# Performance work log

Measured on AMD Instinct MI355X. Metric: run time of the kernel, lower is better.

The kernel has to match this reference:

```python
import jax, jax.numpy as jnp
import numpy as np

B, N, C = 2, 1024, 768
H = 12            # num_heads
HP = 24           # H_prime
HD = C // H       # head_dim = 64
KS = 3            # local conv kernel size
SCALE = HD ** -0.5


def setup_inputs() -> dict:
    key = jax.random.key(0)
    ks = jax.random.split(key, 9)
    s = lambda fan_in: 1.0 / np.sqrt(fan_in)
    return {
        "x": jax.random.normal(ks[0], (B, N, C), jnp.float32),
        "W_qk": jax.random.normal(ks[1], (2 * C, C), jnp.float32) * s(C),
        "W_v": jax.random.normal(ks[2], (C, C), jnp.float32) * s(C),
        "W_exp": jax.random.normal(ks[3], (HP, H), jnp.float32) * s(H),      # 1x1 conv H->HP
        "W_loc": jax.random.normal(ks[4], (HP, 1, KS, KS), jnp.float32) * s(KS * KS),  # depthwise 3x3
        "b_loc": jnp.zeros((HP,), jnp.float32),
        "W_red": jax.random.normal(ks[5], (H, HP), jnp.float32) * s(HP),    # 1x1 conv HP->H
        "W_proj": jax.random.normal(ks[6], (C, C), jnp.float32) * s(C),
        "b_proj": jnp.zeros((C,), jnp.float32),
    }


def _forward(x, W_qk, W_v, W_exp, W_loc, b_loc, W_red, W_proj, b_proj):
    b, n, c = x.shape
    # Attention: qk projection -> (2,B,H,N,HD)
    qk = (x @ W_qk.T).reshape(b, n, 2, H, HD).transpose(2, 0, 3, 1, 4)
    q, k = qk[0], qk[1]                                   # (B,H,N,HD)
    v = (x @ W_v.T).reshape(b, n, H, HD).transpose(0, 2, 1, 3)  # (B,H,N,HD)
    attn = jax.nn.softmax(jnp.einsum('bhnd,bhmd->bhnm', q, k) * SCALE, axis=-1)  # (B,H,N,N)

    # TokenSelector: conv-based reweighting of the attention map
    A_exp = jnp.einsum('oi,binm->bonm', W_exp, attn)      # 1x1 expand -> (B,HP,N,N)
    A_loc = jax.lax.conv_general_dilated(
        A_exp, W_loc, window_strides=(1, 1), padding='SAME',
        dimension_numbers=('NCHW', 'OIHW', 'NCHW'),
        feature_group_count=HP) + b_loc[None, :, None, None]
    A_loc = jax.nn.relu(A_loc)
    A_red = jnp.einsum('oi,binm->bonm', W_red, A_loc) * SCALE  # (B,H,N,N)
    attn2 = jax.nn.softmax(A_red, axis=-1)

    out = jnp.einsum('bhnm,bhmd->bhnd', attn2, v)         # (B,H,N,HD)
    out = out.transpose(0, 2, 1, 3).reshape(b, n, c)      # (B,N,C)
    out = out @ W_proj.T + b_proj
    return out, A_exp


def reference(x, W_qk, W_v, W_exp, W_loc, b_loc, W_red, W_proj, b_proj):
    return _forward(x, W_qk, W_v, W_exp, W_loc, b_loc, W_red, W_proj, b_proj)
```

## Files before the change

kernel.cpp:

```cpp
#include <hip/hip_runtime.h>
#include <math.h>

#define BB    2
#define NN    1024
#define CC    768
#define HH    12
#define HPP   24
#define HD    64
#define SCALE 0.125f

typedef float fvec4 __attribute__((ext_vector_type(4)));

#define SEG   (2*1024*768)
#define QOFF  0
#define KOFF  (SEG)
#define VOFF  (2*SEG)
#define HOFF  (3*SEG)

__global__ __launch_bounds__(256)
void qkv_gemm(const float* __restrict__ x, const float* __restrict__ Wqk,
              const float* __restrict__ Wv, float* __restrict__ ws)
{
    __shared__ float As[16][68];
    __shared__ float Bs[16][68];
    float* qtok = ws + QOFF;
    float* kt   = ws + KOFF;
    float* vws  = ws + VOFF;

    const int tid  = threadIdx.x;
    const int bn   = blockIdx.x;
    const int bm   = blockIdx.y;
    const int tx   = tid & 15, ty = tid >> 4;
    const int lrow = tid >> 2;
    const int lk   = (tid & 3) << 2;

    const int jrow = bn * 64 + lrow;
    const float* Bsrc = (jrow < 1536) ? (Wqk + (size_t)jrow * 768)
                                      : (Wv  + (size_t)(jrow - 1536) * 768);
    const float* Asrc = x + (size_t)(bm * 64 + lrow) * 768;

    float c[4][4] = {};

    for (int k0 = 0; k0 < 768; k0 += 16) {
        float4 av = *(const float4*)(Asrc + k0 + lk);
        float4 bv = *(const float4*)(Bsrc + k0 + lk);
        __syncthreads();
        As[lk+0][lrow] = av.x; As[lk+1][lrow] = av.y;
        As[lk+2][lrow] = av.z; As[lk+3][lrow] = av.w;
        Bs[lk+0][lrow] = bv.x; Bs[lk+1][lrow] = bv.y;
        Bs[lk+2][lrow] = bv.z; Bs[lk+3][lrow] = bv.w;
        __syncthreads();
#pragma unroll
        for (int kk = 0; kk < 16; ++kk) {
            float a[4], b[4];
#pragma unroll
            for (int i = 0; i < 4; ++i) a[i] = As[kk][ty*4 + i];
#pragma unroll
            for (int j = 0; j < 4; ++j) b[j] = Bs[kk][tx*4 + j];
#pragma unroll
            for (int i = 0; i < 4; ++i)
#pragma unroll
                for (int j = 0; j < 4; ++j)
                    c[i][j] = fmaf(a[i], b[j], c[i][j]);
        }
    }

#pragma unroll
    for (int i = 0; i < 4; ++i) {
        const int t = bm*64 + ty*4 + i;
        const int b = t >> 10, n = t & 1023;
#pragma unroll
        for (int j = 0; j < 4; ++j) {
            const int col = bn*64 + tx*4 + j;
            const float val = c[i][j];
            if (col < 768) {
                qtok[(size_t)t*768 + col] = val;
            } else if (col < 1536) {
                const int p = col - 768;
                kt[((size_t)(b*768 + p))*NN + n] = val;
            } else {
                const int p = col - 1536;
                vws[(((size_t)b*HH + (p >> 6))*NN + n)*HD + (p & 63)] = val;
            }
        }
    }
}

__global__ __launch_bounds__(256, 4)
void attn_expand(const float* __restrict__ qtok, const float* __restrict__ kt,
                 const float* __restrict__ Wexp, float* __restrict__ aexp)
{
    __shared__ __align__(16) float qs[2*CC];
    __shared__ float wexp_s[HPP * HH];
    __shared__ float smax[2][HH * 4];
    __shared__ float ssum[2][HH * 4];

    const int tid  = threadIdx.x;
    const int lane = tid & 63, wid = tid >> 6;
    const int x    = blockIdx.x & 7;
    const int b    = x >> 2;
    const int np   = ((x & 3) << 7) | (blockIdx.x >> 3);
    const int n0   = np << 1;
    const int m4   = tid;

    const fvec4* qsrc = (const fvec4*)(qtok + (size_t)(b*NN + n0) * CC);
    ((fvec4*)qs)[tid] = qsrc[tid];
    if (tid < 128) ((fvec4*)qs)[256 + tid] = qsrc[256 + tid];
    for (int i2 = tid; i2 < HPP*HH; i2 += 256) wexp_s[i2] = Wexp[i2];
    __syncthreads();

    fvec4 l0[HH], l1[HH];
#pragma unroll
    for (int h = 0; h < HH; ++h) {
        fvec4 a0 = {0.f,0.f,0.f,0.f}, a1 = {0.f,0.f,0.f,0.f};
        const fvec4* kr = ((const fvec4*)kt) + (size_t)(b*768 + h*64) * 256 + m4;
        const float* q0p = qs + h*64;
        const float* q1p = qs + CC + h*64;
#pragma unroll 8
        for (int d = 0; d < 64; ++d) {
            const fvec4 kv = kr[(size_t)d * 256];
            const float qa = q0p[d];
            const float qb = q1p[d];
            a0.x = fmaf(kv.x, qa, a0.x); a0.y = fmaf(kv.y, qa, a0.y);
            a0.z = fmaf(kv.z, qa, a0.z); a0.w = fmaf(kv.w, qa, a0.w);
            a1.x = fmaf(kv.x, qb, a1.x); a1.y = fmaf(kv.y, qb, a1.y);
            a1.z = fmaf(kv.z, qb, a1.z); a1.w = fmaf(kv.w, qb, a1.w);
        }
        l0[h].x = a0.x*SCALE; l0[h].y = a0.y*SCALE;
        l0[h].z = a0.z*SCALE; l0[h].w = a0.w*SCALE;
        l1[h].x = a1.x*SCALE; l1[h].y = a1.y*SCALE;
        l1[h].z = a1.z*SCALE; l1[h].w = a1.w*SCALE;
    }

#pragma unroll
    for (int h = 0; h < HH; ++h) {
        float t0 = fmaxf(fmaxf(l0[h].x, l0[h].y), fmaxf(l0[h].z, l0[h].w));
        float t1 = fmaxf(fmaxf(l1[h].x, l1[h].y), fmaxf(l1[h].z, l1[h].w));
#pragma unroll
        for (int off = 32; off > 0; off >>= 1) {
            t0 = fmaxf(t0, __shfl_xor(t0, off, 64));
            t1 = fmaxf(t1, __shfl_xor(t1, off, 64));
        }
        if (lane == 0) { smax[0][h*4 + wid] = t0; smax[1][h*4 + wid] = t1; }
    }
    __syncthreads();

#pragma unroll
    for (int h = 0; h < HH; ++h) {
        const float m0 = fmaxf(fmaxf(smax[0][h*4+0], smax[0][h*4+1]),
                               fmaxf(smax[0][h*4+2], smax[0][h*4+3]));
        const float m1 = fmaxf(fmaxf(smax[1][h*4+0], smax[1][h*4+1]),
                               fmaxf(smax[1][h*4+2], smax[1][h*4+3]));
        l0[h].x = __expf(l0[h].x - m0); l0[h].y = __expf(l0[h].y - m0);
        l0[h].z = __expf(l0[h].z - m0); l0[h].w = __expf(l0[h].w - m0);
        l1[h].x = __expf(l1[h].x - m1); l1[h].y = __expf(l1[h].y - m1);
        l1[h].z = __expf(l1[h].z - m1); l1[h].w = __expf(l1[h].w - m1);
        float s0 = (l0[h].x + l0[h].y) + (l0[h].z + l0[h].w);
        float s1 = (l1[h].x + l1[h].y) + (l1[h].z + l1[h].w);
#pragma unroll
        for (int off = 32; off > 0; off >>= 1) {
            s0 += __shfl_xor(s0, off, 64);
            s1 += __shfl_xor(s1, off, 64);
        }
        if (lane == 0) { ssum[0][h*4 + wid] = s0; ssum[1][h*4 + wid] = s1; }
    }
    __syncthreads();

#pragma unroll
    for (int h = 0; h < HH; ++h) {
        const float i0 = 1.f / (ssum[0][h*4+0] + ssum[0][h*4+1] +
                                ssum[0][h*4+2] + ssum[0][h*4+3]);
        const float i1 = 1.f / (ssum[1][h*4+0] + ssum[1][h*4+1] +
                                ssum[1][h*4+2] + ssum[1][h*4+3]);
        l0[h].x *= i0; l0[h].y *= i0; l0[h].z *= i0; l0[h].w *= i0;
        l1[h].x *= i1; l1[h].y *= i1; l1[h].z *= i1; l1[h].w *= i1;
    }

    fvec4* ab = ((fvec4*)aexp) + ((size_t)b*HPP*NN + n0) * 256;
#pragma unroll 4
    for (int o = 0; o < HPP; ++o) {
        fvec4 e0 = {0.f,0.f,0.f,0.f}, e1 = {0.f,0.f,0.f,0.f};
#pragma unroll
        for (int h = 0; h < HH; ++h) {
            const float w = wexp_s[o*HH + h];
            e0.x = fmaf(w, l0[h].x, e0.x); e0.y = fmaf(w, l0[h].y, e0.y);
            e0.z = fmaf(w, l0[h].z, e0.z); e0.w = fmaf(w, l0[h].w, e0.w);
            e1.x = fmaf(w, l1[h].x, e1.x); e1.y = fmaf(w, l1[h].y, e1.y);
            e1.z = fmaf(w, l1[h].z, e1.z); e1.w = fmaf(w, l1[h].w, e1.w);
        }
        fvec4* p0 = ab + (size_t)o * NN * 256 + m4;
        __builtin_nontemporal_store(e0, p0);
        __builtin_nontemporal_store(e1, p0 + 256);
    }
}

__global__ __launch_bounds__(512, 4)
void conv_red_pv(const float* __restrict__ aexp, const float* __restrict__ Wloc,
                 const float* __restrict__ bloc, const float* __restrict__ Wred,
                 const float* __restrict__ vws, float* __restrict__ hout)
{
    __shared__ __align__(16) float probs[8][NN];
    __shared__ float redbuf[2][HH][4];

    const int tid  = threadIdx.x;
    const int lane = tid & 63;
    const int w    = tid >> 6;
    const int tk   = w >> 2;
    const int wq   = w & 3;
    const int t    = tid & 255;

    const int x  = blockIdx.x & 7;
    const int b  = x >> 2;
    const int np = ((x & 3) << 7) | (blockIdx.x >> 3);
    const int n0 = np << 1;
    const int n  = n0 + tk;

    const bool rv0 = n > 0, rv2 = n < NN - 1;

    float4 acc[HH];
#pragma unroll
    for (int i = 0; i < HH; ++i) acc[i] = make_float4(0.f,0.f,0.f,0.f);

    auto loadch = [&](int o, float4 ld[3], float hl[3], float hr[3]) {
        const float* cb = aexp + ((size_t)(b*HPP + o) * NN + (size_t)(n-1)) * NN;
#pragma unroll
        for (int r = 0; r < 3; ++r) {
            const bool ok = (r == 0) ? rv0 : (r == 2 ? rv2 : true);
            const float* rp = cb + (size_t)r * NN;
            if (ok) {
                ld[r] = ((const float4*)rp)[t];
                hl[r] = (lane == 0  && wq > 0) ? rp[4*t - 1] : 0.f;
                hr[r] = (lane == 63 && wq < 3) ? rp[4*t + 4] : 0.f;
            } else {
                ld[r] = make_float4(0.f,0.f,0.f,0.f);
                hl[r] = 0.f; hr[r] = 0.f;
            }
        }
    };

    float4 ld[3]; float hl[3], hr[3];
    loadch(0, ld, hl, hr);

    for (int o = 0; o < HPP; ++o) {
        float4 l2[3]; float h2l[3], h2r[3];
        if (o < HPP-1) loadch(o+1, l2, h2l, h2r);

        const float* wl = Wloc + o*9;
        const float  bb = bloc[o];
        float v0 = bb, v1 = bb, v2 = bb, v3 = bb;
#pragma unroll
        for (int r = 0; r < 3; ++r) {
            const float w0 = wl[r*3+0], w1 = wl[r*3+1], w2 = wl[r*3+2];
            const float4 c = ld[r];
            float lf = __shfl_up(c.w, 1, 64);
            float rt = __shfl_down(c.x, 1, 64);
            if (lane == 0)  lf = hl[r];
            if (lane == 63) rt = hr[r];
            v0 = fmaf(w0, lf,  v0); v0 = fmaf(w1, c.x, v0); v0 = fmaf(w2, c.y, v0);
            v1 = fmaf(w0, c.x, v1); v1 = fmaf(w1, c.y, v1); v1 = fmaf(w2, c.z, v1);
            v2 = fmaf(w0, c.y, v2); v2 = fmaf(w1, c.z, v2); v2 = fmaf(w2, c.w, v2);
            v3 = fmaf(w0, c.z, v3); v3 = fmaf(w1, c.w, v3); v3 = fmaf(w2, rt,  v3);
        }
        v0 = fmaxf(v0, 0.f); v1 = fmaxf(v1, 0.f);
        v2 = fmaxf(v2, 0.f); v3 = fmaxf(v3, 0.f);
#pragma unroll
        for (int i = 0; i < HH; ++i) {
            const float wr = Wred[i*HPP + o];
            acc[i].x = fmaf(wr, v0, acc[i].x);
            acc[i].y = fmaf(wr, v1, acc[i].y);
            acc[i].z = fmaf(wr, v2, acc[i].z);
            acc[i].w = fmaf(wr, v3, acc[i].w);
        }
        if (o < HPP-1) {
#pragma unroll
            for (int r = 0; r < 3; ++r) { ld[r]=l2[r]; hl[r]=h2l[r]; hr[r]=h2r[r]; }
        }
    }
#pragma unroll
    for (int i = 0; i < HH; ++i) {
        acc[i].x *= SCALE; acc[i].y *= SCALE;
        acc[i].z *= SCALE; acc[i].w *= SCALE;
    }

#pragma unroll
    for (int i = 0; i < HH; ++i) {
        float tm = fmaxf(fmaxf(acc[i].x, acc[i].y), fmaxf(acc[i].z, acc[i].w));
#pragma unroll
        for (int off = 32; off > 0; off >>= 1) tm = fmaxf(tm, __shfl_xor(tm, off, 64));
        if (lane == 0) redbuf[tk][i][wq] = tm;
    }
    __syncthreads();
    float mh[HH];
#pragma unroll
    for (int i = 0; i < HH; ++i)
        mh[i] = fmaxf(fmaxf(redbuf[tk][i][0], redbuf[tk][i][1]),
                      fmaxf(redbuf[tk][i][2], redbuf[tk][i][3]));
    __syncthreads();

#pragma unroll
    for (int i = 0; i < HH; ++i) {
        acc[i].x = __expf(acc[i].x - mh[i]);
        acc[i].y = __expf(acc[i].y - mh[i]);
        acc[i].z = __expf(acc[i].z - mh[i]);
        acc[i].w = __expf(acc[i].w - mh[i]);
        float s = (acc[i].x + acc[i].y) + (acc[i].z + acc[i].w);
#pragma unroll
        for (int off = 32; off > 0; off >>= 1) s += __shfl_xor(s, off, 64);
        if (lane == 0) redbuf[tk][i][wq] = s;
    }
    __syncthreads();
#pragma unroll
    for (int i = 0; i < HH; ++i) {
        const float inv = 1.f / (redbuf[tk][i][0] + redbuf[tk][i][1] +
                                 redbuf[tk][i][2] + redbuf[tk][i][3]);
        acc[i].x *= inv; acc[i].y *= inv; acc[i].z *= inv; acc[i].w *= inv;
    }

    const int hq = w >> 1;
    const int dh = w & 1;
    const int mg = lane >> 3;
    const int dq = lane & 7;

    for (int g = 0; g < 3; ++g) {
        __syncthreads();
#pragma unroll
        for (int q2 = 0; q2 < 4; ++q2)
            ((float4*)&probs[q2*2 + tk][0])[t] = acc[4*g + q2];
        __syncthreads();

        const int h = 4*g + hq;
        const float4* vp = ((const float4*)vws)
                         + ((size_t)(b*HH + h) * NN) * 16 + dh*8 + dq;
        const float* p0 = &probs[hq*2 + 0][0] + mg;
        const float* p1 = &probs[hq*2 + 1][0] + mg;
        float4 a0 = make_float4(0.f,0.f,0.f,0.f);
        float4 a1 = make_float4(0.f,0.f,0.f,0.f);
#pragma unroll 8
        for (int m0 = 0; m0 < NN; m0 += 8) {
            const float  pa = p0[m0];
            const float  pb = p1[m0];
            const float4 vv = vp[(size_t)(m0 + mg) * 16];
            a0.x = fmaf(pa, vv.x, a0.x); a0.y = fmaf(pa, vv.y, a0.y);
            a0.z = fmaf(pa, vv.z, a0.z); a0.w = fmaf(pa, vv.w, a0.w);
            a1.x = fmaf(pb, vv.x, a1.x); a1.y = fmaf(pb, vv.y, a1.y);
            a1.z = fmaf(pb, vv.z, a1.z); a1.w = fmaf(pb, vv.w, a1.w);
        }
#pragma unroll
        for (int off = 8; off < 64; off <<= 1) {
            a0.x += __shfl_xor(a0.x, off, 64); a0.y += __shfl_xor(a0.y, off, 64);
            a0.z += __shfl_xor(a0.z, off, 64); a0.w += __shfl_xor(a0.w, off, 64);
            a1.x += __shfl_xor(a1.x, off, 64); a1.y += __shfl_xor(a1.y, off, 64);
            a1.z += __shfl_xor(a1.z, off, 64); a1.w += __shfl_xor(a1.w, off, 64);
        }
        if (mg == 0) {
            ((float4*)(hout + ((size_t)(b*NN + n0    ) * CC) + h*HD))[dh*8 + dq] = a0;
            ((float4*)(hout + ((size_t)(b*NN + n0 + 1) * CC) + h*HD))[dh*8 + dq] = a1;
        }
    }
}

__global__ __launch_bounds__(256)
void proj_gemm(const float* __restrict__ A, const float* __restrict__ Wp,
               const float* __restrict__ bias, float* __restrict__ out)
{
    __shared__ float As[16][68];
    __shared__ float Bs[16][68];

    const int tid  = threadIdx.x;
    const int bn   = blockIdx.x;
    const int bm   = blockIdx.y;
    const int tx   = tid & 15, ty = tid >> 4;
    const int lrow = tid >> 2;
    const int lk   = (tid & 3) << 2;

    const float* Asrc = A  + (size_t)(bm*64 + lrow) * 768;
    const float* Bsrc = Wp + (size_t)(bn*64 + lrow) * 768;

    float c[4][4] = {};

    for (int k0 = 0; k0 < 768; k0 += 16) {
        float4 av = *(const float4*)(Asrc + k0 + lk);
        float4 bv = *(const float4*)(Bsrc + k0 + lk);
        __syncthreads();
        As[lk+0][lrow] = av.x; As[lk+1][lrow] = av.y;
        As[lk+2][lrow] = av.z; As[lk+3][lrow] = av.w;
        Bs[lk+0][lrow] = bv.x; Bs[lk+1][lrow] = bv.y;
        Bs[lk+2][lrow] = bv.z; Bs[lk+3][lrow] = bv.w;
        __syncthreads();
#pragma unroll
        for (int kk = 0; kk < 16; ++kk) {
            float a[4], b[4];
#pragma unroll
            for (int i = 0; i < 4; ++i) a[i] = As[kk][ty*4 + i];
#pragma unroll
            for (int j = 0; j < 4; ++j) b[j] = Bs[kk][tx*4 + j];
#pragma unroll
            for (int i = 0; i < 4; ++i)
#pragma unroll
                for (int j = 0; j < 4; ++j)
                    c[i][j] = fmaf(a[i], b[j], c[i][j]);
        }
    }

#pragma unroll
    for (int i = 0; i < 4; ++i) {
        const int t = bm*64 + ty*4 + i;
#pragma unroll
        for (int j = 0; j < 4; ++j) {
            const int col = bn*64 + tx*4 + j;
            out[(size_t)t*768 + col] = c[i][j] + bias[col];
        }
    }
}

extern "C" void kernel_launch(void* const* d_in, const int* in_sizes, int n_in,
                              void* d_out, int out_size, void* d_ws, size_t ws_size,
                              hipStream_t stream)
{
    const float* x     = (const float*)d_in[0];
    const float* Wqk   = (const float*)d_in[1];
    const float* Wv    = (const float*)d_in[2];
    const float* Wexp  = (const float*)d_in[3];
    const float* Wloc  = (const float*)d_in[4];
    const float* bloc  = (const float*)d_in[5];
    const float* Wred  = (const float*)d_in[6];
    const float* Wproj = (const float*)d_in[7];
    const float* bproj = (const float*)d_in[8];

    float* out  = (float*)d_out;
    float* aexp = out + (size_t)SEG;
    float* ws   = (float*)d_ws;

    qkv_gemm   <<<dim3(36, 32), 256, 0, stream>>>(x, Wqk, Wv, ws);
    attn_expand<<<dim3(BB * NN / 2), 256, 0, stream>>>(ws + QOFF, ws + KOFF, Wexp, aexp);
    conv_red_pv<<<dim3(BB * NN / 2), 512, 0, stream>>>(aexp, Wloc, bloc, Wred,
                                                       ws + VOFF, ws + HOFF);
    proj_gemm  <<<dim3(12, 32), 256, 0, stream>>>(ws + HOFF, Wproj, bproj, out);
}
```

Before: 768.9 us.

## Enlarge GEMM tiles to 128x64 with double-buffered LDS and vector stores

```diff
diff --git a/kernel.cpp b/kernel.cpp
--- a/kernel.cpp
+++ b/kernel.cpp
@@ -17,76 +17,109 @@
 #define VOFF  (2*SEG)
 #define HOFF  (3*SEG)
 
+#define ASTR 132
+#define BSTR 68
+
 __global__ __launch_bounds__(256)
 void qkv_gemm(const float* __restrict__ x, const float* __restrict__ Wqk,
               const float* __restrict__ Wv, float* __restrict__ ws)
 {
-    __shared__ float As[16][68];
-    __shared__ float Bs[16][68];
+    __shared__ float As[2][16*ASTR];
+    __shared__ float Bs[2][16*BSTR];
     float* qtok = ws + QOFF;
     float* kt   = ws + KOFF;
     float* vws  = ws + VOFF;
 
-    const int tid  = threadIdx.x;
-    const int bn   = blockIdx.x;
-    const int bm   = blockIdx.y;
-    const int tx   = tid & 15, ty = tid >> 4;
-    const int lrow = tid >> 2;
-    const int lk   = (tid & 3) << 2;
-
-    const int jrow = bn * 64 + lrow;
-    const float* Bsrc = (jrow < 1536) ? (Wqk + (size_t)jrow * 768)
-                                      : (Wv  + (size_t)(jrow - 1536) * 768);
-    const float* Asrc = x + (size_t)(bm * 64 + lrow) * 768;
-
-    float c[4][4] = {};
-
-    for (int k0 = 0; k0 < 768; k0 += 16) {
-        float4 av = *(const float4*)(Asrc + k0 + lk);
-        float4 bv = *(const float4*)(Bsrc + k0 + lk);
+    const int tid = threadIdx.x;
+    const int bn  = blockIdx.x;
+    const int bm  = blockIdx.y;
+    const int tx  = tid & 15, ty = tid >> 4;
+
+    const int am  = tid >> 1, ak = (tid & 1) * 8;
+    const int bnr = tid >> 2, bk = (tid & 3) * 4;
+
+    const float* Ap = x + (size_t)(bm*128 + am) * 768 + ak;
+    const int jrow  = bn*64 + bnr;
+    const float* Bp = (jrow < 1536) ? (Wqk + (size_t)jrow * 768 + bk)
+                                    : (Wv  + (size_t)(jrow - 1536) * 768 + bk);
+
+    float acc[8][4] = {};
+
+    float4 a0 = *(const float4*)(Ap);
+    float4 a1 = *(const float4*)(Ap + 4);
+    float4 bv = *(const float4*)(Bp);
+#pragma unroll
+    for (int j = 0; j < 4; ++j) {
+        As[0][(ak+j)*ASTR + am]   = ((const float*)&a0)[j];
+        As[0][(ak+4+j)*ASTR + am] = ((const float*)&a1)[j];
+        Bs[0][(bk+j)*BSTR + bnr]  = ((const float*)&bv)[j];
+    }
+    __syncthreads();
+
+    for (int t = 0; t < 48; ++t) {
+        const int cur = t & 1;
+        if (t < 47) {
+            a0 = *(const float4*)(Ap + (t+1)*16);
+            a1 = *(const float4*)(Ap + (t+1)*16 + 4);
+            bv = *(const float4*)(Bp + (t+1)*16);
+        }
+        const float* Asb = As[cur];
+        const float* Bsb = Bs[cur];
+#pragma unroll
+        for (int kk = 0; kk < 16; ++kk) {
+            float a[8], b[4];
+#pragma unroll
+            for (int i = 0; i < 8; ++i) a[i] = Asb[kk*ASTR + ty*8 + i];
+#pragma unroll
+            for (int j = 0; j < 4; ++j) b[j] = Bsb[kk*BSTR + tx*4 + j];
+#pragma unroll
+            for (int i = 0; i < 8; ++i)
+#pragma unroll
+                for (int j = 0; j < 4; ++j)
+                    acc[i][j] = fmaf(a[i], b[j], acc[i][j]);
+        }
+        if (t < 47) {
+#pragma unroll
+            for (int j = 0; j < 4; ++j) {
+                As[cur^1][(ak+j)*ASTR + am]   = ((const float*)&a0)[j];
+                As[cur^1][(ak+4+j)*ASTR + am] = ((const float*)&a1)[j];
+                Bs[cur^1][(bk+j)*BSTR + bnr]  = ((const float*)&bv)[j];
+            }
+        }
         __syncthreads();
-        As[lk+0][lrow] = av.x; As[lk+1][lrow] = av.y;
-        As[lk+2][lrow] = av.z; As[lk+3][lrow] = av.w;
-        Bs[lk+0][lrow] = bv.x; Bs[lk+1][lrow] = bv.y;
-        Bs[lk+2][lrow] = bv.z; Bs[lk+3][lrow] = bv.w;
-        __syncthreads();
-#pragma unroll
-        for (int kk = 0; kk < 16; ++kk) {
-            float a[4], b[4];
-#pragma unroll
-            for (int i = 0; i < 4; ++i) a[i] = As[kk][ty*4 + i];
-#pragma unroll
-            for (int j = 0; j < 4; ++j) b[j] = Bs[kk][tx*4 + j];
-#pragma unroll
-            for (int i = 0; i < 4; ++i)
-#pragma unroll
-                for (int j = 0; j < 4; ++j)
-                    c[i][j] = fmaf(a[i], b[j], c[i][j]);
-        }
-    }
-
-#pragma unroll
-    for (int i = 0; i < 4; ++i) {
-        const int t = bm*64 + ty*4 + i;
-        const int b = t >> 10, n = t & 1023;
-#pragma unroll
-        for (int j = 0; j < 4; ++j) {
-            const int col = bn*64 + tx*4 + j;
-            const float val = c[i][j];
-            if (col < 768) {
-                qtok[(size_t)t*768 + col] = val;
-            } else if (col < 1536) {
-                const int p = col - 768;
-                kt[((size_t)(b*768 + p))*NN + n] = val;
-            } else {
-                const int p = col - 1536;
-                vws[(((size_t)b*HH + (p >> 6))*NN + n)*HD + (p & 63)] = val;
-            }
+    }
+
+    const int colbase = bn*64 + tx*4;
+    if (colbase < 768) {
+#pragma unroll
+        for (int i = 0; i < 8; ++i) {
+            const int trow = bm*128 + ty*8 + i;
+            float4 o = {acc[i][0], acc[i][1], acc[i][2], acc[i][3]};
+            *(float4*)(qtok + (size_t)trow*768 + colbase) = o;
+        }
+    } else if (colbase < 1536) {
+        const int p = colbase - 768;
+#pragma unroll
+        for (int i = 0; i < 8; ++i) {
+            const int trow = bm*128 + ty*8 + i;
+            const int b = trow >> 10, n = trow & 1023;
+#pragma unroll
+            for (int j = 0; j < 4; ++j)
+                kt[((size_t)(b*768 + p + j))*NN + n] = acc[i][j];
+        }
+    } else {
+        const int p = colbase - 1536;
+#pragma unroll
+        for (int i = 0; i < 8; ++i) {
+            const int trow = bm*128 + ty*8 + i;
+            const int b = trow >> 10, n = trow & 1023;
+            float4 o = {acc[i][0], acc[i][1], acc[i][2], acc[i][3]};
+            *(float4*)(vws + (((size_t)b*HH + (p >> 6))*NN + n)*HD + (p & 63)) = o;
         }
     }
 }
 
-__global__ __launch_bounds__(256, 4)
+__global__ __launch_bounds__(256, 2)
 void attn_expand(const float* __restrict__ qtok, const float* __restrict__ kt,
                  const float* __restrict__ Wexp, float* __restrict__ aexp)
 {
@@ -194,7 +227,7 @@
     }
 }
 
-__global__ __launch_bounds__(512, 4)
+__global__ __launch_bounds__(512, 2)
 void conv_red_pv(const float* __restrict__ aexp, const float* __restrict__ Wloc,
                  const float* __restrict__ bloc, const float* __restrict__ Wred,
                  const float* __restrict__ vws, float* __restrict__ hout)
@@ -363,53 +396,74 @@
 void proj_gemm(const float* __restrict__ A, const float* __restrict__ Wp,
                const float* __restrict__ bias, float* __restrict__ out)
 {
-    __shared__ float As[16][68];
-    __shared__ float Bs[16][68];
-
-    const int tid  = threadIdx.x;
-    const int bn   = blockIdx.x;
-    const int bm   = blockIdx.y;
-    const int tx   = tid & 15, ty = tid >> 4;
-    const int lrow = tid >> 2;
-    const int lk   = (tid & 3) << 2;
-
-    const float* Asrc = A  + (size_t)(bm*64 + lrow) * 768;
-    const float* Bsrc = Wp + (size_t)(bn*64 + lrow) * 768;
-
-    float c[4][4] = {};
-
-    for (int k0 = 0; k0 < 768; k0 += 16) {
-        float4 av = *(const float4*)(Asrc + k0 + lk);
-        float4 bv = *(const float4*)(Bsrc + k0 + lk);
+    __shared__ float As[2][16*ASTR];
+    __shared__ float Bs[2][16*BSTR];
+
+    const int tid = threadIdx.x;
+    const int bn  = blockIdx.x;
+    const int bm  = blockIdx.y;
+    const int tx  = tid & 15, ty = tid >> 4;
+
+    const int am  = tid >> 1, ak = (tid & 1) * 8;
+    const int bnr = tid >> 2, bk = (tid & 3) * 4;
+
+    const float* Ap = A  + (size_t)(bm*128 + am) * 768 + ak;
+    const float* Bp = Wp + (size_t)(bn*64 + bnr) * 768 + bk;
+
+    float acc[8][4] = {};
+
+    float4 a0 = *(const float4*)(Ap);
+    float4 a1 = *(const float4*)(Ap + 4);
+    float4 bv = *(const float4*)(Bp);
+#pragma unroll
+    for (int j = 0; j < 4; ++j) {
+        As[0][(ak+j)*ASTR + am]   = ((const float*)&a0)[j];
+        As[0][(ak+4+j)*ASTR + am] = ((const float*)&a1)[j];
+        Bs[0][(bk+j)*BSTR + bnr]  = ((const float*)&bv)[j];
+    }
+    __syncthreads();
+
+    for (int t = 0; t < 48; ++t) {
+        const int cur = t & 1;
+        if (t < 47) {
+            a0 = *(const float4*)(Ap + (t+1)*16);
+            a1 = *(const float4*)(Ap + (t+1)*16 + 4);
+            bv = *(const float4*)(Bp + (t+1)*16);
+        }
+        const float* Asb = As[cur];
+        const float* Bsb = Bs[cur];
+#pragma unroll
+        for (int kk = 0; kk < 16; ++kk) {
+            float a[8], b[4];
+#pragma unroll
+            for (int i = 0; i < 8; ++i) a[i] = Asb[kk*ASTR + ty*8 + i];
+#pragma unroll
+            for (int j = 0; j < 4; ++j) b[j] = Bsb[kk*BSTR + tx*4 + j];
+#pragma unroll
+            for (int i = 0; i < 8; ++i)
+#pragma unroll
+                for (int j = 0; j < 4; ++j)
+                    acc[i][j] = fmaf(a[i], b[j], acc[i][j]);
+        }
+        if (t < 47) {
+#pragma unroll
+            for (int j = 0; j < 4; ++j) {
+                As[cur^1][(ak+j)*ASTR + am]   = ((const float*)&a0)[j];
+                As[cur^1][(ak+4+j)*ASTR + am] = ((const float*)&a1)[j];
+                Bs[cur^1][(bk+j)*BSTR + bnr]  = ((const float*)&bv)[j];
+            }
+        }
         __syncthreads();
-        As[lk+0][lrow] = av.x; As[lk+1][lrow] = av.y;
-        As[lk+2][lrow] = av.z; As[lk+3][lrow] = av.w;
-        Bs[lk+0][lrow] = bv.x; Bs[lk+1][lrow] = bv.y;
-        Bs[lk+2][lrow] = bv.z; Bs[lk+3][lrow] = bv.w;
-        __syncthreads();
-#pragma unroll
-        for (int kk = 0; kk < 16; ++kk) {
-            float a[4], b[4];
-#pragma unroll
-            for (int i = 0; i < 4; ++i) a[i] = As[kk][ty*4 + i];
-#pragma unroll
-            for (int j = 0; j < 4; ++j) b[j] = Bs[kk][tx*4 + j];
-#pragma unroll
-            for (int i = 0; i < 4; ++i)
-#pragma unroll
-                for (int j = 0; j < 4; ++j)
-                    c[i][j] = fmaf(a[i], b[j], c[i][j]);
-        }
-    }
-
-#pragma unroll
-    for (int i = 0; i < 4; ++i) {
-        const int t = bm*64 + ty*4 + i;
-#pragma unroll
-        for (int j = 0; j < 4; ++j) {
-            const int col = bn*64 + tx*4 + j;
-            out[(size_t)t*768 + col] = c[i][j] + bias[col];
-        }
+    }
+
+    const int colbase = bn*64 + tx*4;
+    const float4 bb = *(const float4*)(bias + colbase);
+#pragma unroll
+    for (int i = 0; i < 8; ++i) {
+        const int trow = bm*128 + ty*8 + i;
+        float4 o = {acc[i][0] + bb.x, acc[i][1] + bb.y,
+                    acc[i][2] + bb.z, acc[i][3] + bb.w};
+        *(float4*)(out + (size_t)trow*768 + colbase) = o;
     }
 }
 
@@ -431,9 +485,9 @@
     float* aexp = out + (size_t)SEG;
     float* ws   = (float*)d_ws;
 
-    qkv_gemm   <<<dim3(36, 32), 256, 0, stream>>>(x, Wqk, Wv, ws);
+    qkv_gemm   <<<dim3(36, 16), 256, 0, stream>>>(x, Wqk, Wv, ws);
     attn_expand<<<dim3(BB * NN / 2), 256, 0, stream>>>(ws + QOFF, ws + KOFF, Wexp, aexp);
     conv_red_pv<<<dim3(BB * NN / 2), 512, 0, stream>>>(aexp, Wloc, bloc, Wred,
                                                        ws + VOFF, ws + HOFF);
-    proj_gemm  <<<dim3(12, 32), 256, 0, stream>>>(ws + HOFF, Wproj, bproj, out);
+    proj_gemm  <<<dim3(12, 16), 256, 0, stream>>>(ws + HOFF, Wproj, bproj, out);
 }
```

New measurement: 757.0 us. About the same (-1.5%).
